# Optimization experiments

Hardware: AMD Instinct MI355X
Metric: run time of the kernel (lower is better)

The kernel has to match this reference:

```python
import jax, jax.numpy as jnp
import numpy as np

D = 1024       # d_model
S = 32         # n_slots
EMA = 0.05     # slot_ema (alpha)
RSCALE = 1.0   # read_logit_scale
LN_EPS = 1e-5


def setup_inputs() -> dict:
    key = jax.random.key(0)
    ks = jax.random.split(key, 6)
    B, T = 2, 2048
    h = jax.random.normal(ks[0], (B, T, D), jnp.float32)
    # init_batched_memory_state: small random slots
    state0 = jax.random.normal(ks[1], (B, S, D), jnp.float32) * 0.01
    # xavier_uniform for (out=D, in=D) Linear weights, zero bias
    bound = float(np.sqrt(6.0 / (D + D)))
    Wq = jax.random.uniform(ks[2], (D, D), jnp.float32, -bound, bound)
    Wv = jax.random.uniform(ks[3], (D, D), jnp.float32, -bound, bound)
    bq = jnp.zeros((D,), jnp.float32)
    bv = jnp.zeros((D,), jnp.float32)
    ln_gamma = jnp.ones((D,), jnp.float32)
    ln_beta = jnp.zeros((D,), jnp.float32)
    return {"h": h, "state0": state0, "ln_gamma": ln_gamma, "ln_beta": ln_beta,
            "Wq": Wq, "bq": bq, "Wv": Wv, "bv": bv, "chunk_size": 128}


def _layer_norm(x, gamma, beta):
    mu = jnp.mean(x, axis=-1, keepdims=True)
    var = jnp.mean(jnp.square(x - mu), axis=-1, keepdims=True)
    return (x - mu) * jax.lax.rsqrt(var + LN_EPS) * gamma + beta


def reference(h, state0, ln_gamma, ln_beta, Wq, bq, Wv, bv, chunk_size):
    """write_parallel (soft-routed EMA prefix-scan write) followed by
    read_parallel (per-token softmax slot attention). Returns (ctx, final_state)."""
    B, T, d = h.shape
    alpha = EMA
    a = 1.0 - alpha
    h_norm = _layer_norm(h, ln_gamma, ln_beta)                  # (B,T,d)
    v = h_norm @ Wv.T + bv                                      # value_proj
    q = h_norm @ Wq.T + bq                                      # query_proj
    scale = RSCALE * d ** (-0.5)
    # routing weights from queries vs initial state (breaks seq dependency)
    scores = jnp.einsum('btd,bsd->bts', q, state0) * scale       # (B,T,S)
    w = jax.nn.softmax(scores, axis=-1)
    u = alpha * w[..., None] * v[:, :, None, :]                  # (B,T,S,d)

    n_chunks = T // chunk_size
    Cn = chunk_size
    u_chunks = u.reshape(B, n_chunks, Cn, S, d).transpose(1, 0, 2, 3, 4)
    t_idx = jnp.arange(Cn, dtype=h.dtype)
    decay = a ** t_idx                                           # (Cn,)
    inv_decay = 1.0 / jnp.clip(decay, 1e-30)
    t1_decay = a ** (t_idx + 1.0)

    def step(state, u_c):  # state (B,S,d), u_c (B,Cn,S,d)
        cs = jnp.cumsum(u_c * inv_decay[None, :, None, None], axis=1)
        chunk_states = (decay[None, :, None, None] * cs
                        + t1_decay[None, :, None, None] * state[:, None])
        return chunk_states[:, -1], chunk_states

    final_state, states = jax.lax.scan(step, state0, u_chunks)
    states = states.transpose(1, 0, 2, 3, 4).reshape(B, T, S, d)  # (B,T,S,d)

    # read_parallel: softmax slot attention per token against its own state
    scores_r = jnp.einsum('btd,btsd->bts', q, states) * scale
    attn = jax.nn.softmax(scores_r, axis=-1)
    ctx = jnp.einsum('bts,btsd->btd', attn, states)               # (B,T,d)
    return ctx, final_state
```

## Files before the change

### kernel.cpp

```cpp
#include <hip/hip_runtime.h>

#define Bn 2
#define Tn 2048
#define Dn 1024
#define Sn 32
#define CH 64
#define NCH 32
#define ALPHA 0.05f
#define Adec 0.95f
#define SCALE 0.03125f

typedef __attribute__((ext_vector_type(8))) __bf16 bf16x8;
typedef __attribute__((ext_vector_type(4))) __bf16 bf16x4;
typedef __attribute__((ext_vector_type(4))) float f32x4;

__device__ __forceinline__ void async_copy16(const void* g, void* l) {
  __builtin_amdgcn_global_load_lds(
      (const __attribute__((address_space(1))) unsigned int*)g,
      (__attribute__((address_space(3))) unsigned int*)l, 16, 0, 0);
}

__device__ __forceinline__ bool is_bf16(const void* gam) {
  return ((const unsigned short*)gam)[0] == 0x3F80u;
}

#define W8 (Dn * Dn / 8)
#define S8 (Bn * Sn * Dn / 8)
#define LNB (Bn * Tn)
__global__ __launch_bounds__(256) void prep_k(
    const void* __restrict__ hp, const void* __restrict__ gp, const void* __restrict__ bp,
    const void* __restrict__ Wq, const void* __restrict__ Wv, const void* __restrict__ s0,
    __bf16* __restrict__ hn, __bf16* __restrict__ Wqb, __bf16* __restrict__ Wvb,
    __bf16* __restrict__ s0b) {
  bool isb = is_bf16(gp);
  int tid = threadIdx.x;
  if (blockIdx.x >= LNB) {
    int g = (blockIdx.x - LNB) * 256 + tid;
    const void* src; __bf16* dst; int off;
    if (g < W8)            { src = Wq; dst = Wqb; off = g; }
    else if (g < 2 * W8)   { src = Wv; dst = Wvb; off = g - W8; }
    else                   { src = s0; dst = s0b; off = g - 2 * W8; }
    if (isb) {
      *(bf16x8*)&dst[(size_t)off * 8] = ((const bf16x8*)src)[off];
    } else {
      const float* s = (const float*)src + (size_t)off * 8;
      f32x4 a = *(const f32x4*)s, b = *(const f32x4*)(s + 4);
      bf16x8 t;
      t[0] = (__bf16)a[0]; t[1] = (__bf16)a[1]; t[2] = (__bf16)a[2]; t[3] = (__bf16)a[3];
      t[4] = (__bf16)b[0]; t[5] = (__bf16)b[1]; t[6] = (__bf16)b[2]; t[7] = (__bf16)b[3];
      *(bf16x8*)&dst[(size_t)off * 8] = t;
    }
    return;
  }
  int row = blockIdx.x;
  float x0, x1, x2, x3;
  if (isb) {
    const __bf16* x = (const __bf16*)hp + (size_t)row * Dn;
    bf16x4 xv = *(const bf16x4*)&x[tid * 4];
    x0 = (float)xv[0]; x1 = (float)xv[1]; x2 = (float)xv[2]; x3 = (float)xv[3];
  } else {
    const float* x = (const float*)hp + (size_t)row * Dn;
    f32x4 xv = *(const f32x4*)&x[tid * 4];
    x0 = xv[0]; x1 = xv[1]; x2 = xv[2]; x3 = xv[3];
  }
  float s  = x0 + x1 + x2 + x3;
  float s2 = x0*x0 + x1*x1 + x2*x2 + x3*x3;
  #pragma unroll
  for (int m = 32; m >= 1; m >>= 1) { s += __shfl_xor(s, m); s2 += __shfl_xor(s2, m); }
  __shared__ float red[8];
  int wave = tid >> 6, lane = tid & 63;
  if (lane == 0) { red[wave] = s; red[4 + wave] = s2; }
  __syncthreads();
  s  = red[0] + red[1] + red[2] + red[3];
  s2 = red[4] + red[5] + red[6] + red[7];
  float mu  = s * (1.0f / Dn);
  float var = s2 * (1.0f / Dn) - mu * mu;
  float rs  = rsqrtf(var + 1e-5f);
  float g0, g1, g2, g3, be0, be1, be2, be3;
  if (isb) {
    bf16x4 gv = *(const bf16x4*)&((const __bf16*)gp)[tid * 4];
    bf16x4 bv = *(const bf16x4*)&((const __bf16*)bp)[tid * 4];
    g0 = (float)gv[0]; g1 = (float)gv[1]; g2 = (float)gv[2]; g3 = (float)gv[3];
    be0 = (float)bv[0]; be1 = (float)bv[1]; be2 = (float)bv[2]; be3 = (float)bv[3];
  } else {
    f32x4 gv = *(const f32x4*)&((const float*)gp)[tid * 4];
    f32x4 bv = *(const f32x4*)&((const float*)bp)[tid * 4];
    g0 = gv[0]; g1 = gv[1]; g2 = gv[2]; g3 = gv[3];
    be0 = bv[0]; be1 = bv[1]; be2 = bv[2]; be3 = bv[3];
  }
  bf16x4 o;
  o[0] = (__bf16)((x0 - mu) * rs * g0 + be0);
  o[1] = (__bf16)((x1 - mu) * rs * g1 + be1);
  o[2] = (__bf16)((x2 - mu) * rs * g2 + be2);
  o[3] = (__bf16)((x3 - mu) * rs * g3 + be3);
  *(bf16x4*)&hn[(size_t)row * Dn + tid * 4] = o;
}

__global__ __launch_bounds__(256) void gemm_qv_k(
    const __bf16* __restrict__ A,
    const __bf16* __restrict__ Wqb, const void* __restrict__ bqp,
    const __bf16* __restrict__ Wvb, const void* __restrict__ bvp,
    const void* __restrict__ gam,
    __bf16* __restrict__ Qo, __bf16* __restrict__ Vo) {
  const int K = Dn, N = Dn;
  bool isb = is_bf16(gam);
  int mt = blockIdx.x & 31;
  int ng = blockIdx.x >> 5;
  const __bf16* W; const void* biasp; __bf16* O; int nt;
  if (ng < 8) { W = Wqb; biasp = bqp; O = Qo; nt = ng; }
  else        { W = Wvb; biasp = bvp; O = Vo; nt = ng - 8; }
  int m0 = mt * 128, n0 = nt * 128;
  __shared__ alignas(16) __bf16 lA[128 * 64];
  __shared__ alignas(16) __bf16 lB[128 * 64];
  int tid = threadIdx.x, lane = tid & 63, wave = tid >> 6;
  int wm = (wave >> 1) * 64, wn = (wave & 1) * 64;
  int lm = lane & 15, q8 = (lane >> 4) * 8;
  f32x4 zero4 = {0.f, 0.f, 0.f, 0.f};
  f32x4 acc[4][4];
  #pragma unroll
  for (int i = 0; i < 4; ++i)
    #pragma unroll
    for (int j = 0; j < 4; ++j) acc[i][j] = zero4;

  for (int k0 = 0; k0 < K; k0 += 64) {
    __syncthreads();
    #pragma unroll
    for (int r = 0; r < 4; ++r) {
      int idx = r * 256 + tid;
      int row = idx >> 3, c8 = (idx & 7) * 8;
      async_copy16(&A[(size_t)(m0 + row) * K + k0 + c8], &lA[idx * 8]);
      async_copy16(&W[(size_t)(n0 + row) * K + k0 + c8], &lB[idx * 8]);
    }
    __syncthreads();
    #pragma unroll
    for (int kk = 0; kk < 64; kk += 32) {
      bf16x8 af[4], bfr[4];
      #pragma unroll
      for (int i = 0; i < 4; ++i) {
        af[i]  = *(const bf16x8*)&lA[(wm + i * 16 + lm) * 64 + kk + q8];
        bfr[i] = *(const bf16x8*)&lB[(wn + i * 16 + lm) * 64 + kk + q8];
      }
      #pragma unroll
      for (int i = 0; i < 4; ++i)
        #pragma unroll
        for (int j = 0; j < 4; ++j)
          acc[i][j] = __builtin_amdgcn_mfma_f32_16x16x32_bf16(af[i], bfr[j], acc[i][j], 0, 0, 0);
    }
  }
  int r4 = (lane >> 4) * 4;
  #pragma unroll
  for (int j = 0; j < 4; ++j) {
    int colN = n0 + wn + j * 16 + lm;
    float bb = isb ? (float)((const __bf16*)biasp)[colN] : ((const float*)biasp)[colN];
    #pragma unroll
    for (int i = 0; i < 4; ++i) {
      int row0 = m0 + wm + i * 16 + r4;
      #pragma unroll
      for (int r = 0; r < 4; ++r)
        O[(size_t)(row0 + r) * N + colN] = (__bf16)(acc[i][j][r] + bb);
    }
  }
}

__global__ __launch_bounds__(256) void router_k(const __bf16* __restrict__ qb,
    const __bf16* __restrict__ s0b, float* __restrict__ wbuf) {
  int tokBase = blockIdx.x * 16;
  int b = tokBase >> 11;
  int tid = threadIdx.x, lane = tid & 63, wave = tid >> 6;
  int lm = lane & 15, q8 = (lane >> 4) * 8;
  const __bf16* qrow = qb + (size_t)(tokBase + lm) * Dn + q8;
  const __bf16* s0r  = s0b + ((size_t)b * Sn + lm) * Dn + q8;
  const __bf16* s1r  = s0r + (size_t)16 * Dn;
  f32x4 zero4 = {0.f, 0.f, 0.f, 0.f};
  f32x4 acc0 = zero4, acc1 = zero4;
  #pragma unroll
  for (int ks = 0; ks < 8; ++ks) {
    int k0 = wave * 256 + ks * 32;
    bf16x8 af = *(const bf16x8*)&qrow[k0];
    bf16x8 b0 = *(const bf16x8*)&s0r[k0];
    bf16x8 b1 = *(const bf16x8*)&s1r[k0];
    acc0 = __builtin_amdgcn_mfma_f32_16x16x32_bf16(af, b0, acc0, 0, 0, 0);
    acc1 = __builtin_amdgcn_mfma_f32_16x16x32_bf16(af, b1, acc1, 0, 0, 0);
  }
  __shared__ float red[4][16][33];
  int r4 = (lane >> 4) * 4;
  #pragma unroll
  for (int r = 0; r < 4; ++r) {
    red[wave][r4 + r][lm]      = acc0[r];
    red[wave][r4 + r][lm + 16] = acc1[r];
  }
  __syncthreads();
  int t = tid >> 4, s = tid & 15;
  float sc0 = (red[0][t][s]      + red[1][t][s])      + (red[2][t][s]      + red[3][t][s]);
  float sc1 = (red[0][t][s + 16] + red[1][t][s + 16]) + (red[2][t][s + 16] + red[3][t][s + 16]);
  sc0 *= SCALE; sc1 *= SCALE;
  float mx = fmaxf(sc0, sc1);
  #pragma unroll
  for (int m = 8; m >= 1; m >>= 1) mx = fmaxf(mx, __shfl_xor(mx, m));
  float e0 = __expf(sc0 - mx), e1 = __expf(sc1 - mx);
  float su = e0 + e1;
  #pragma unroll
  for (int m = 8; m >= 1; m >>= 1) su += __shfl_xor(su, m);
  float inv = 1.f / su;
  wbuf[(size_t)(tokBase + t) * Sn + s]      = e0 * inv;
  wbuf[(size_t)(tokBase + t) * Sn + s + 16] = e1 * inv;
}

__global__ __launch_bounds__(256) void contrib_k(const __bf16* __restrict__ v,
    const float* __restrict__ wbuf, float* __restrict__ contrib) {
  int blk = blockIdx.x;
  int bc = blk >> 2, dq = blk & 3;
  int b = bc >> 5, c = bc & 31;
  int tokBase = b * Tn + c * CH;
  int d0 = dq * 256;
  __shared__ alignas(16) float coef[CH * Sn];
  __shared__ float dp[CH];
  int tid = threadIdx.x;
  if (tid < CH) dp[tid] = powf(Adec, (float)(CH - 1 - tid));
  __syncthreads();
  for (int i = tid; i < CH * Sn; i += 256) {
    int j = i >> 5;
    coef[i] = ALPHA * dp[j] * wbuf[(size_t)tokBase * Sn + i];
  }
  __syncthreads();
  int st = tid >> 6;
  int dg = tid & 63;
  int d4 = d0 + dg * 4;
  int sb = st * 8;
  f32x4 zero4 = {0.f, 0.f, 0.f, 0.f};
  f32x4 acc[8];
  #pragma unroll
  for (int i = 0; i < 8; ++i) acc[i] = zero4;
  for (int j = 0; j < CH; ++j) {
    bf16x4 vv = *(const bf16x4*)&v[(size_t)(tokBase + j) * Dn + d4];
    f32x4 vf = {(float)vv[0], (float)vv[1], (float)vv[2], (float)vv[3]};
    f32x4 c0 = *(const f32x4*)&coef[j * Sn + sb];
    f32x4 c1 = *(const f32x4*)&coef[j * Sn + sb + 4];
    acc[0] += vf * c0[0]; acc[1] += vf * c0[1]; acc[2] += vf * c0[2]; acc[3] += vf * c0[3];
    acc[4] += vf * c1[0]; acc[5] += vf * c1[1]; acc[6] += vf * c1[2]; acc[7] += vf * c1[3];
  }
  float* outp = contrib + (size_t)bc * Sn * Dn;
  #pragma unroll
  for (int i = 0; i < 8; ++i)
    *(f32x4*)&outp[(size_t)(sb + i) * Dn + d4] = acc[i];
}

__global__ __launch_bounds__(256) void scan_k(const void* __restrict__ s0p,
    const float* __restrict__ contrib, const void* __restrict__ gam,
    __bf16* __restrict__ S0b, void* __restrict__ outp) {
  int idx = blockIdx.x * 256 + threadIdx.x;
  bool isb = is_bf16(gam);
  int b = idx >> 15, sd = idx & 32767;
  float val = isb ? (float)((const __bf16*)s0p)[idx] : ((const float*)s0p)[idx];
  const float aC = powf(Adec, (float)CH);
  float cv[NCH];
  #pragma unroll
  for (int c = 0; c < NCH; ++c)
    cv[c] = contrib[((size_t)(b * NCH + c) << 15) + sd];
  #pragma unroll
  for (int c = 0; c < NCH; ++c) {
    S0b[((size_t)(b * NCH + c) << 15) + sd] = (__bf16)val;
    val = aC * val + cv[c];
  }
  size_t fsbase = (size_t)Bn * Tn * Dn;
  if (isb) ((__bf16*)outp)[fsbase + idx] = (__bf16)val;
  else     ((float*)outp)[fsbase + idx] = val;
}

__global__ __launch_bounds__(256) void attn_k(
    const __bf16* __restrict__ q, const __bf16* __restrict__ v,
    const float* __restrict__ wbuf, const __bf16* __restrict__ S0b,
    float* __restrict__ Pbuf, float* __restrict__ A2buf) {
  int bc = blockIdx.x;
  int b = bc >> 5, c = bc & 31;
  int tokBase = b * Tn + c * CH;
  const __bf16* S0c = S0b + (size_t)bc * Sn * Dn;

  __shared__ alignas(16) __bf16 lQ[CH * 64];
  __shared__ alignas(16) __bf16 lV[CH * 64];
  __shared__ alignas(16) __bf16 lS[Sn * 64];
  __shared__ alignas(16) __bf16 lM[CH * 72];
  __shared__ alignas(16) __bf16 lW[CH * 40];
  __shared__ alignas(16) __bf16 lWt[Sn * 72];
  __shared__ alignas(16) __bf16 lAt[CH * 40];
  __shared__ float dp[CH + 1];

  int tid = threadIdx.x, lane = tid & 63, wave = tid >> 6;
  int lm = lane & 15, q8 = (lane >> 4) * 8;
  int r4 = (lane >> 4) * 4;
  f32x4 zero4 = {0.f, 0.f, 0.f, 0.f};
  f32x4 aQV[4], aQS[2];
  #pragma unroll
  for (int i = 0; i < 4; ++i) aQV[i] = zero4;
  aQS[0] = zero4; aQS[1] = zero4;

  for (int i = tid; i < CH * Sn; i += 256) {
    int j = i >> 5, s = i & 31;
    __bf16 wb = (__bf16)wbuf[(size_t)tokBase * Sn + i];
    lW[j * 40 + s] = wb;
    lWt[s * 72 + j] = wb;
  }
  if (tid < CH + 1) dp[tid] = powf(Adec, (float)tid);

  for (int k0 = 0; k0 < Dn; k0 += 64) {
    __syncthreads();
    #pragma unroll
    for (int r = 0; r < 2; ++r) {
      int idx = r * 256 + tid;
      int row = idx >> 3, c8 = (idx & 7) * 8;
      async_copy16(&q[(size_t)(tokBase + row) * Dn + k0 + c8], &lQ[idx * 8]);
      async_copy16(&v[(size_t)(tokBase + row) * Dn + k0 + c8], &lV[idx * 8]);
    }
    async_copy16(&S0c[(size_t)(tid >> 3) * Dn + k0 + (tid & 7) * 8], &lS[tid * 8]);
    __syncthreads();
    #pragma unroll
    for (int kk = 0; kk < 64; kk += 32) {
      bf16x8 af = *(const bf16x8*)&lQ[(wave * 16 + lm) * 64 + kk + q8];
      #pragma unroll
      for (int j = 0; j < 4; ++j) {
        bf16x8 bb = *(const bf16x8*)&lV[(j * 16 + lm) * 64 + kk + q8];
        aQV[j] = __builtin_amdgcn_mfma_f32_16x16x32_bf16(af, bb, aQV[j], 0, 0, 0);
      }
      #pragma unroll
      for (int j = 0; j < 2; ++j) {
        bf16x8 bb = *(const bf16x8*)&lS[(j * 16 + lm) * 64 + kk + q8];
        aQS[j] = __builtin_amdgcn_mfma_f32_16x16x32_bf16(af, bb, aQS[j], 0, 0, 0);
      }
    }
  }

  #pragma unroll
  for (int jt = 0; jt < 4; ++jt)
    #pragma unroll
    for (int r = 0; r < 4; ++r) {
      int t = wave * 16 + r4 + r, j = jt * 16 + lm;
      float f = (j <= t) ? ALPHA * dp[t - j] : 0.0f;
      lM[t * 72 + j] = (__bf16)(aQV[jt][r] * f);
    }

  f32x4 sc[2]; sc[0] = zero4; sc[1] = zero4;
  #pragma unroll
  for (int kt = 0; kt < 2; ++kt) {
    bf16x8 am = *(const bf16x8*)&lM[(wave * 16 + lm) * 72 + kt * 32 + q8];
    #pragma unroll
    for (int st = 0; st < 2; ++st) {
      bf16x8 bb = *(const bf16x8*)&lWt[(st * 16 + lm) * 72 + kt * 32 + q8];
      sc[st] = __builtin_amdgcn_mfma_f32_16x16x32_bf16(am, bb, sc[st], 0, 0, 0);
    }
  }
  float at0[4], at1[4];
  #pragma unroll
  for (int r = 0; r < 4; ++r) {
    int t = wave * 16 + r4 + r;
    float aQ = dp[t + 1];
    float s0v = SCALE * (aQ * aQS[0][r] + sc[0][r]);
    float s1v = SCALE * (aQ * aQS[1][r] + sc[1][r]);
    float mx = fmaxf(s0v, s1v);
    #pragma unroll
    for (int m = 8; m >= 1; m >>= 1) mx = fmaxf(mx, __shfl_xor(mx, m));
    float e0 = __expf(s0v - mx), e1 = __expf(s1v - mx);
    float su = e0 + e1;
    #pragma unroll
    for (int m = 8; m >= 1; m >>= 1) su += __shfl_xor(su, m);
    float inv = 1.f / su;
    at0[r] = e0 * inv; at1[r] = e1 * inv;
    A2buf[(size_t)bc * CH * Sn + t * Sn + lm]      = aQ * at0[r];
    A2buf[(size_t)bc * CH * Sn + t * Sn + 16 + lm] = aQ * at1[r];
    lAt[t * 40 + lm]      = (__bf16)at0[r];
    lAt[t * 40 + 16 + lm] = (__bf16)at1[r];
  }
  bf16x8 aa = *(const bf16x8*)&lAt[(wave * 16 + lm) * 40 + q8];
  #pragma unroll
  for (int jt = 0; jt < 4; ++jt) {
    bf16x8 bb = *(const bf16x8*)&lW[(jt * 16 + lm) * 40 + q8];
    f32x4 pj = __builtin_amdgcn_mfma_f32_16x16x32_bf16(aa, bb, zero4, 0, 0, 0);
    #pragma unroll
    for (int r = 0; r < 4; ++r) {
      int t = wave * 16 + r4 + r, j = jt * 16 + lm;
      float val = (j <= t) ? ALPHA * dp[t - j] * pj[r] : 0.0f;
      Pbuf[(size_t)bc * CH * CH + t * CH + j] = val;
    }
  }
}

__global__ __launch_bounds__(256) void ctx_k(const __bf16* __restrict__ v,
    const __bf16* __restrict__ S0b, const float* __restrict__ Pbuf,
    const float* __restrict__ A2buf, const void* __restrict__ gam,
    void* __restrict__ ctxp) {
  int blk = blockIdx.x;
  int bc = blk >> 3, dt = blk & 7;
  int b = bc >> 5, c = bc & 31;
  int tokBase = b * Tn + c * CH;
  int d0 = dt * 128;
  bool isb = is_bf16(gam);
  __shared__ alignas(16) float lP[CH * CH];
  __shared__ alignas(16) float lA2[CH * Sn];
  __shared__ alignas(16) __bf16 lV[CH * 128];
  __shared__ alignas(16) __bf16 lS[Sn * 128];
  int tid = threadIdx.x;
  {
    const f32x4* src = (const f32x4*)(Pbuf + (size_t)bc * CH * CH);
    f32x4* dst = (f32x4*)lP;
    for (int i = tid; i < CH * CH / 4; i += 256) dst[i] = src[i];
    const f32x4* src2 = (const f32x4*)(A2buf + (size_t)bc * CH * Sn);
    f32x4* dst2 = (f32x4*)lA2;
    for (int i = tid; i < CH * Sn / 4; i += 256) dst2[i] = src2[i];
    for (int i = tid; i < CH * 128 / 8; i += 256) {
      int j = i >> 4, dd = (i & 15) * 8;
      *(bf16x8*)&lV[j * 128 + dd] = *(const bf16x8*)&v[(size_t)(tokBase + j) * Dn + d0 + dd];
    }
    for (int i = tid; i < Sn * 128 / 8; i += 256) {
      int s = i >> 4, dd = (i & 15) * 8;
      *(bf16x8*)&lS[s * 128 + dd] = *(const bf16x8*)&S0b[((size_t)bc * Sn + s) * Dn + d0 + dd];
    }
  }
  __syncthreads();
  int tt = tid >> 5, dg = tid & 31;
  int t0 = tt * 8, d4 = dg * 4;
  f32x4 zero4 = {0.f, 0.f, 0.f, 0.f};
  f32x4 acc[8];
  #pragma unroll
  for (int i = 0; i < 8; ++i) acc[i] = zero4;
  for (int j4 = 0; j4 < CH; j4 += 4) {
    f32x4 vf[4];
    #pragma unroll
    for (int k = 0; k < 4; ++k) {
      bf16x4 vv = *(const bf16x4*)&lV[(j4 + k) * 128 + d4];
      vf[k] = f32x4{(float)vv[0], (float)vv[1], (float)vv[2], (float)vv[3]};
    }
    #pragma unroll
    for (int i = 0; i < 8; ++i) {
      f32x4 pr = *(const f32x4*)&lP[(t0 + i) * CH + j4];
      acc[i] += vf[0] * pr[0]; acc[i] += vf[1] * pr[1];
      acc[i] += vf[2] * pr[2]; acc[i] += vf[3] * pr[3];
    }
  }
  for (int s4 = 0; s4 < Sn; s4 += 4) {
    f32x4 sf[4];
    #pragma unroll
    for (int k = 0; k < 4; ++k) {
      bf16x4 sv = *(const bf16x4*)&lS[(s4 + k) * 128 + d4];
      sf[k] = f32x4{(float)sv[0], (float)sv[1], (float)sv[2], (float)sv[3]};
    }
    #pragma unroll
    for (int i = 0; i < 8; ++i) {
      f32x4 ar = *(const f32x4*)&lA2[(t0 + i) * Sn + s4];
      acc[i] += sf[0] * ar[0]; acc[i] += sf[1] * ar[1];
      acc[i] += sf[2] * ar[2]; acc[i] += sf[3] * ar[3];
    }
  }
  if (isb) {
    __bf16* ctx = (__bf16*)ctxp;
    #pragma unroll
    for (int i = 0; i < 8; ++i) {
      bf16x4 o;
      o[0] = (__bf16)acc[i][0]; o[1] = (__bf16)acc[i][1];
      o[2] = (__bf16)acc[i][2]; o[3] = (__bf16)acc[i][3];
      *(bf16x4*)&ctx[(size_t)(tokBase + t0 + i) * Dn + d0 + d4] = o;
    }
  } else {
    float* ctx = (float*)ctxp;
    #pragma unroll
    for (int i = 0; i < 8; ++i)
      *(f32x4*)&ctx[(size_t)(tokBase + t0 + i) * Dn + d0 + d4] = acc[i];
  }
}

extern "C" void kernel_launch(void* const* d_in, const int* in_sizes, int n_in,
                              void* d_out, int out_size, void* d_ws, size_t ws_size,
                              hipStream_t stream) {
  (void)in_sizes; (void)n_in; (void)out_size; (void)ws_size;
  const void* h      = d_in[0];
  const void* state0 = d_in[1];
  const void* gam    = d_in[2];
  const void* bet    = d_in[3];
  const void* Wq     = d_in[4];
  const void* bq     = d_in[5];
  const void* Wv     = d_in[6];
  const void* bv     = d_in[7];

  char* ws = (char*)d_ws;
  __bf16* hn      = (__bf16*)(ws);
  __bf16* qb      = (__bf16*)(ws + (8u << 20));
  __bf16* vb      = (__bf16*)(ws + (16u << 20));
  float*  wbuf    = (float*)(ws + (24u << 20));
  float*  contrib = (float*)(ws + (25u << 20));
  __bf16* S0b     = (__bf16*)(ws + (34u << 20));
  float*  Pbuf    = (float*)(ws + (43u << 20));
  float*  A2buf   = (float*)(ws + (45u << 20));
  __bf16* Wqb     = (__bf16*)(ws + (47u << 20));
  __bf16* Wvb     = (__bf16*)(ws + (49u << 20));
  __bf16* s0b     = (__bf16*)(ws + (51u << 20));

  int convBlocks = (2 * W8 + S8) / 256;
  prep_k<<<LNB + convBlocks, 256, 0, stream>>>(h, gam, bet, Wq, Wv, state0,
                                               hn, Wqb, Wvb, s0b);
  gemm_qv_k<<<512, 256, 0, stream>>>(hn, Wqb, bq, Wvb, bv, gam, qb, vb);
  router_k<<<Bn * Tn / 16, 256, 0, stream>>>(qb, s0b, wbuf);
  contrib_k<<<Bn * NCH * 4, 256, 0, stream>>>(vb, wbuf, contrib);
  scan_k<<<Bn * Sn * Dn / 256, 256, 0, stream>>>(state0, contrib, gam, S0b, d_out);
  attn_k<<<Bn * NCH, 256, 0, stream>>>(qb, vb, wbuf, S0b, Pbuf, A2buf);
  ctx_k<<<Bn * NCH * 8, 256, 0, stream>>>(vb, S0b, Pbuf, A2buf, gam, d_out);
}
```

Before: 176.6 us.

## Share A tile across Q/V projections and keep whole Q chunk resident in LDS

Result: no change. 177.8 us (+0.7%).

```diff
diff --git a/kernel.cpp b/kernel.cpp
--- a/kernel.cpp
+++ b/kernel.cpp
@@ -104,16 +104,14 @@
     __bf16* __restrict__ Qo, __bf16* __restrict__ Vo) {
   const int K = Dn, N = Dn;
   bool isb = is_bf16(gam);
-  int mt = blockIdx.x & 31;
-  int ng = blockIdx.x >> 5;
-  const __bf16* W; const void* biasp; __bf16* O; int nt;
-  if (ng < 8) { W = Wqb; biasp = bqp; O = Qo; nt = ng; }
-  else        { W = Wvb; biasp = bvp; O = Vo; nt = ng - 8; }
-  int m0 = mt * 128, n0 = nt * 128;
-  __shared__ alignas(16) __bf16 lA[128 * 64];
-  __shared__ alignas(16) __bf16 lB[128 * 64];
+  int mt = blockIdx.x & 63;
+  int nt = blockIdx.x >> 6;
+  int m0 = mt * 64, n0 = nt * 128;
+  __shared__ alignas(16) __bf16 lA[64 * 64];
+  __shared__ alignas(16) __bf16 lBq[128 * 64];
+  __shared__ alignas(16) __bf16 lBv[128 * 64];
   int tid = threadIdx.x, lane = tid & 63, wave = tid >> 6;
-  int wm = (wave >> 1) * 64, wn = (wave & 1) * 64;
+  int isv = wave >> 1, wn = (wave & 1) * 64;
   int lm = lane & 15, q8 = (lane >> 4) * 8;
   f32x4 zero4 = {0.f, 0.f, 0.f, 0.f};
   f32x4 acc[4][4];
@@ -125,19 +123,26 @@
   for (int k0 = 0; k0 < K; k0 += 64) {
     __syncthreads();
     #pragma unroll
+    for (int r = 0; r < 2; ++r) {
+      int idx = r * 256 + tid;
+      int row = idx >> 3, c8 = (idx & 7) * 8;
+      async_copy16(&A[(size_t)(m0 + row) * K + k0 + c8], &lA[idx * 8]);
+    }
+    #pragma unroll
     for (int r = 0; r < 4; ++r) {
       int idx = r * 256 + tid;
       int row = idx >> 3, c8 = (idx & 7) * 8;
-      async_copy16(&A[(size_t)(m0 + row) * K + k0 + c8], &lA[idx * 8]);
-      async_copy16(&W[(size_t)(n0 + row) * K + k0 + c8], &lB[idx * 8]);
+      async_copy16(&Wqb[(size_t)(n0 + row) * K + k0 + c8], &lBq[idx * 8]);
+      async_copy16(&Wvb[(size_t)(n0 + row) * K + k0 + c8], &lBv[idx * 8]);
     }
     __syncthreads();
+    const __bf16* lB = isv ? lBv : lBq;
     #pragma unroll
     for (int kk = 0; kk < 64; kk += 32) {
       bf16x8 af[4], bfr[4];
       #pragma unroll
       for (int i = 0; i < 4; ++i) {
-        af[i]  = *(const bf16x8*)&lA[(wm + i * 16 + lm) * 64 + kk + q8];
+        af[i]  = *(const bf16x8*)&lA[(i * 16 + lm) * 64 + kk + q8];
         bfr[i] = *(const bf16x8*)&lB[(wn + i * 16 + lm) * 64 + kk + q8];
       }
       #pragma unroll
@@ -147,6 +152,8 @@
           acc[i][j] = __builtin_amdgcn_mfma_f32_16x16x32_bf16(af[i], bfr[j], acc[i][j], 0, 0, 0);
     }
   }
+  const void* biasp = isv ? bvp : bqp;
+  __bf16* O = isv ? Vo : Qo;
   int r4 = (lane >> 4) * 4;
   #pragma unroll
   for (int j = 0; j < 4; ++j) {
@@ -154,7 +161,7 @@
     float bb = isb ? (float)((const __bf16*)biasp)[colN] : ((const float*)biasp)[colN];
     #pragma unroll
     for (int i = 0; i < 4; ++i) {
-      int row0 = m0 + wm + i * 16 + r4;
+      int row0 = m0 + i * 16 + r4;
       #pragma unroll
       for (int r = 0; r < 4; ++r)
         O[(size_t)(row0 + r) * N + colN] = (__bf16)(acc[i][j][r] + bb);
@@ -276,14 +283,15 @@
   int tokBase = b * Tn + c * CH;
   const __bf16* S0c = S0b + (size_t)bc * Sn * Dn;
 
-  __shared__ alignas(16) __bf16 lQ[CH * 64];
-  __shared__ alignas(16) __bf16 lV[CH * 64];
-  __shared__ alignas(16) __bf16 lS[Sn * 64];
-  __shared__ alignas(16) __bf16 lM[CH * 72];
-  __shared__ alignas(16) __bf16 lW[CH * 40];
-  __shared__ alignas(16) __bf16 lWt[Sn * 72];
-  __shared__ alignas(16) __bf16 lAt[CH * 40];
-  __shared__ float dp[CH + 1];
+  __shared__ alignas(16) __bf16 lQ[CH * Dn];
+  __shared__ alignas(16) char ovl[28 * 1024];
+  __bf16* lV = (__bf16*)ovl;
+  __bf16* lS = (__bf16*)(ovl + 8192);
+  __bf16* lM  = (__bf16*)ovl;
+  __bf16* lW  = (__bf16*)(ovl + 9216);
+  __bf16* lWt = (__bf16*)(ovl + 14336);
+  __bf16* lAt = (__bf16*)(ovl + 18944);
+  float*  dp  = (float*)(ovl + 24064);
 
   int tid = threadIdx.x, lane = tid & 63, wave = tid >> 6;
   int lm = lane & 15, q8 = (lane >> 4) * 8;
@@ -294,28 +302,25 @@
   for (int i = 0; i < 4; ++i) aQV[i] = zero4;
   aQS[0] = zero4; aQS[1] = zero4;
 
-  for (int i = tid; i < CH * Sn; i += 256) {
-    int j = i >> 5, s = i & 31;
-    __bf16 wb = (__bf16)wbuf[(size_t)tokBase * Sn + i];
-    lW[j * 40 + s] = wb;
-    lWt[s * 72 + j] = wb;
+  #pragma unroll
+  for (int r = 0; r < 32; ++r) {
+    int idx = r * 256 + tid;
+    async_copy16(&q[(size_t)(tokBase + (idx >> 7)) * Dn + (idx & 127) * 8], &lQ[idx * 8]);
   }
   if (tid < CH + 1) dp[tid] = powf(Adec, (float)tid);
 
   for (int k0 = 0; k0 < Dn; k0 += 64) {
-    __syncthreads();
-    #pragma unroll
-    for (int r = 0; r < 2; ++r) {
-      int idx = r * 256 + tid;
+    {
+      int idx = tid;
       int row = idx >> 3, c8 = (idx & 7) * 8;
-      async_copy16(&q[(size_t)(tokBase + row) * Dn + k0 + c8], &lQ[idx * 8]);
       async_copy16(&v[(size_t)(tokBase + row) * Dn + k0 + c8], &lV[idx * 8]);
+      async_copy16(&v[(size_t)(tokBase + 32 + row) * Dn + k0 + c8], &lV[(256 + idx) * 8]);
     }
     async_copy16(&S0c[(size_t)(tid >> 3) * Dn + k0 + (tid & 7) * 8], &lS[tid * 8]);
     __syncthreads();
     #pragma unroll
     for (int kk = 0; kk < 64; kk += 32) {
-      bf16x8 af = *(const bf16x8*)&lQ[(wave * 16 + lm) * 64 + kk + q8];
+      bf16x8 af = *(const bf16x8*)&lQ[(wave * 16 + lm) * Dn + k0 + kk + q8];
       #pragma unroll
       for (int j = 0; j < 4; ++j) {
         bf16x8 bb = *(const bf16x8*)&lV[(j * 16 + lm) * 64 + kk + q8];
@@ -327,8 +332,15 @@
         aQS[j] = __builtin_amdgcn_mfma_f32_16x16x32_bf16(af, bb, aQS[j], 0, 0, 0);
       }
     }
-  }
-
+    __syncthreads();
+  }
+
+  for (int i = tid; i < CH * Sn; i += 256) {
+    int j = i >> 5, s = i & 31;
+    __bf16 wb = (__bf16)wbuf[(size_t)tokBase * Sn + i];
+    lW[j * 40 + s] = wb;
+    lWt[s * 72 + j] = wb;
+  }
   #pragma unroll
   for (int jt = 0; jt < 4; ++jt)
     #pragma unroll
@@ -337,6 +349,7 @@
       float f = (j <= t) ? ALPHA * dp[t - j] : 0.0f;
       lM[t * 72 + j] = (__bf16)(aQV[jt][r] * f);
     }
+  __syncthreads();
 
   f32x4 sc[2]; sc[0] = zero4; sc[1] = zero4;
   #pragma unroll
```
